# Kernel optimization log

Measured on AMD Instinct MI355X. Metric: run time of the kernel, lower is better.

The kernel has to match this reference:

```python
import jax, jax.numpy as jnp
import numpy as np

B, S, H, NH, L, ML = 4, 2048, 768, 8, 128, 15
DH = H // NH
PERIOD = 16  # newline every 16 tokens -> 15 content tokens per line


def _layernorm(x, g, b, eps=1e-5):
    m = x.mean(-1, keepdims=True)
    v = ((x - m) ** 2).mean(-1, keepdims=True)
    return (x - m) / jnp.sqrt(v + eps) * g + b


def setup_inputs() -> dict:
    key = jax.random.key(0)
    ks = jax.random.split(key, 8)
    sc = 0.02
    return {
        "hidden": jax.random.normal(ks[0], (B, S, H), jnp.float32),
        "in_proj_w": jax.random.normal(ks[1], (3 * H, H), jnp.float32) * sc,
        "in_proj_b": jnp.zeros((3 * H,), jnp.float32),
        "out_proj_w": jax.random.normal(ks[2], (H, H), jnp.float32) * sc,
        "out_proj_b": jnp.zeros((H,), jnp.float32),
        "W1": jax.random.normal(ks[3], (H, 2 * H), jnp.float32) * sc,
        "b1": jnp.zeros((H,), jnp.float32),
        "g1": jnp.ones((H,), jnp.float32),
        "be1": jnp.zeros((H,), jnp.float32),
        "W2": jax.random.normal(ks[4], (H, H), jnp.float32) * sc,
        "b2": jnp.zeros((H,), jnp.float32),
        "g2": jnp.ones((H,), jnp.float32),
        "be2": jnp.zeros((H,), jnp.float32),
        "W3": jax.random.normal(ks[5], (1, H), jnp.float32) * sc,
        "b3": jnp.zeros((1,), jnp.float32),
        # padded ragged line structure (what the torch loops derive from newline positions)
        "line_starts": jnp.tile(jnp.arange(L, dtype=jnp.int32) * PERIOD, (B, 1)),  # [B,L]
        "line_lens": jnp.full((B, L), ML, jnp.int32),                              # [B,L]
        "context_len": jnp.full((B,), S, jnp.int32),                               # [B]
    }


def reference(hidden, in_proj_w, in_proj_b, out_proj_w, out_proj_b,
              W1, b1, g1, be1, W2, b2, g2, be2, W3, b3,
              line_starts, line_lens, context_len):
    # --- gather per-line tokens into a padded [B, L, ML, H] block ---
    pos = line_starts[:, :, None] + jnp.arange(ML, dtype=line_starts.dtype)      # [B,L,ML]
    tok_mask = jnp.arange(ML)[None, None, :] < line_lens[:, :, None]             # [B,L,ML]
    pos_c = jnp.clip(pos, 0, S - 1)
    bidx = jnp.arange(B)[:, None, None]
    line_tok = hidden[bidx, pos_c]                                               # [B,L,ML,H]

    # --- nn.MultiheadAttention: query=line tokens, key/value=global context ---
    Wq, Wk, Wv = jnp.split(in_proj_w, 3, axis=0)
    bq, bk, bv = jnp.split(in_proj_b, 3, axis=0)
    q = (line_tok @ Wq.T + bq).reshape(B, L, ML, NH, DH)
    k = (hidden @ Wk.T + bk).reshape(B, S, NH, DH)
    v = (hidden @ Wv.T + bv).reshape(B, S, NH, DH)

    scale = 1.0 / np.float32(np.sqrt(DH))
    scores = jnp.einsum('blmhd,bshd->blhms', q, k) * scale                       # [B,L,NH,ML,S]
    kmask = jnp.arange(S)[None, :] < context_len[:, None]                        # [B,S]
    scores = jnp.where(kmask[:, None, None, None, :], scores, -1e9)
    attn = jax.nn.softmax(scores, axis=-1)
    o = jnp.einsum('blhms,bshd->blmhd', attn, v).reshape(B, L, ML, H)
    o = o @ out_proj_w.T + out_proj_b                                            # [B,L,ML,H]

    # --- masked mean-pool over the line's tokens ---
    m = tok_mask[..., None].astype(hidden.dtype)
    denom = jnp.maximum(line_lens, 1)[..., None].astype(hidden.dtype)            # [B,L,1]
    line_mean = (line_tok * m).sum(2) / denom                                    # [B,L,H]
    attn_mean = (o * m).sum(2) / denom                                           # [B,L,H]

    # --- classifier: Linear -> LN -> GELU -> Residual(Linear->LN->GELU) -> Linear ---
    x = jnp.concatenate([line_mean, attn_mean], axis=-1)                         # [B,L,2H]
    x = jax.nn.gelu(_layernorm(x @ W1.T + b1, g1, be1), approximate=False)
    x = x + jax.nn.gelu(_layernorm(x @ W2.T + b2, g2, be2), approximate=False)
    logits = (x @ W3.T + b3)[..., 0]                                             # [B,L]

    # empty lines get logit -10 (as in the torch loop)
    logits = jnp.where(line_lens > 0, logits, jnp.asarray(-10.0, logits.dtype))
    return jax.nn.sigmoid(logits)
```

## Files before the change

kernel.cpp:

```cpp
#include <hip/hip_runtime.h>
#include <hip/hip_bf16.h>
#include <cmath>

using bf16 = __hip_bfloat16;
typedef __attribute__((ext_vector_type(8))) short short8;
typedef __attribute__((ext_vector_type(4))) short s16x4;
typedef __attribute__((ext_vector_type(4))) float f32x4;

#define B_   4
#define S_   2048
#define H_   768
#define H2_  1536
#define H3_  2304
#define NH_  8
#define DH_  96
#define L_   128
#define ML_  15
#define LG_  8
#define QR_  128
#define CH_  32
#define NS_  2
#define SLC_ (S_ / NS_)
#define ELD  36
#define VTLD 56
#define KLD  104
#define VTR  112

__device__ __forceinline__ float gelu_exact(float v) {
    return 0.5f * v * (1.0f + erff(v * 0.7071067811865475f));
}
__device__ __forceinline__ short f2bs(float f) {
    bf16 h = __float2bfloat16(f);
    return *reinterpret_cast<short*>(&h);
}
__device__ __forceinline__ short8 ld_frag8(const short* p) {
    union { short8 v; s16x4 h[2]; } u;
    u.h[0] = *(const s16x4*)p;
    u.h[1] = *(const s16x4*)(p + 4);
    return u.v;
}

__global__ __launch_bounds__(256) void f2b_k(
    const float* __restrict__ src, bf16* __restrict__ dst, int n)
{
    const int i = (blockIdx.x * 256 + threadIdx.x) * 8;
    if (i >= n) return;
    float4 a = *(const float4*)(src + i);
    float4 b = *(const float4*)(src + i + 4);
    short8 r;
    r[0] = f2bs(a.x); r[1] = f2bs(a.y); r[2] = f2bs(a.z); r[3] = f2bs(a.w);
    r[4] = f2bs(b.x); r[5] = f2bs(b.y); r[6] = f2bs(b.z); r[7] = f2bs(b.w);
    *(short8*)(dst + i) = r;
}

template <typename T>
__device__ __forceinline__ void stage8(const T* src, bf16* dst);
template <>
__device__ __forceinline__ void stage8<bf16>(const bf16* src, bf16* dst) {
    *(int4*)dst = *(const int4*)src;
}
template <>
__device__ __forceinline__ void stage8<float>(const float* src, bf16* dst) {
    float4 a = *(const float4*)src;
    float4 b = *(const float4*)(src + 4);
    short8 r;
    r[0] = f2bs(a.x); r[1] = f2bs(a.y); r[2] = f2bs(a.z); r[3] = f2bs(a.w);
    r[4] = f2bs(b.x); r[5] = f2bs(b.y); r[6] = f2bs(b.z); r[7] = f2bs(b.w);
    *(short8*)dst = r;
}

__global__ __launch_bounds__(256) void gemm128_bt(
    const bf16* __restrict__ A, const bf16* __restrict__ Bm,
    const float* __restrict__ bias, bf16* __restrict__ C,
    int M, int N, int K, int ldc)
{
    __shared__ alignas(16) bf16 As[128 * 32];
    __shared__ alignas(16) bf16 Bs[128 * 32];
    const int t = threadIdx.x;
    const int wave = t >> 6, lane = t & 63;
    const int l15 = lane & 15, quad = lane >> 4;
    const int m0 = blockIdx.x * 128, n0 = blockIdx.y * 128;
    const int wm = wave & 1, wn = wave >> 1;
    const int srow = t >> 1, scol = (t & 1) * 16;

    const bf16* aP = A + (size_t)(m0 + srow) * K + scol;
    const bf16* bP = Bm + (size_t)(n0 + srow) * K + scol;
    bf16* aL = &As[srow * 32 + scol];
    bf16* bL = &Bs[srow * 32 + scol];

    f32x4 acc[4][4];
#pragma unroll
    for (int i = 0; i < 4; i++)
#pragma unroll
        for (int j = 0; j < 4; j++) acc[i][j] = (f32x4){0.f, 0.f, 0.f, 0.f};

    for (int k0 = 0; k0 < K; k0 += 32) {
        int4 ra0 = *(const int4*)(aP + k0);
        int4 ra1 = *(const int4*)(aP + k0 + 8);
        int4 rb0 = *(const int4*)(bP + k0);
        int4 rb1 = *(const int4*)(bP + k0 + 8);
        __syncthreads();
        *(int4*)aL = ra0; *(int4*)(aL + 8) = ra1;
        *(int4*)bL = rb0; *(int4*)(bL + 8) = rb1;
        __syncthreads();
        short8 af[4], bfq[4];
#pragma unroll
        for (int i = 0; i < 4; i++)
            af[i] = *(const short8*)&As[(wm * 64 + i * 16 + l15) * 32 + quad * 8];
#pragma unroll
        for (int j = 0; j < 4; j++)
            bfq[j] = *(const short8*)&Bs[(wn * 64 + j * 16 + l15) * 32 + quad * 8];
#pragma unroll
        for (int i = 0; i < 4; i++)
#pragma unroll
            for (int j = 0; j < 4; j++)
                acc[i][j] = __builtin_amdgcn_mfma_f32_16x16x32_bf16(af[i], bfq[j], acc[i][j], 0, 0, 0);
    }

#pragma unroll
    for (int j = 0; j < 4; j++) {
        const int col = n0 + wn * 64 + j * 16 + l15;
        const float bv = bias[col];
#pragma unroll
        for (int i = 0; i < 4; i++) {
            const int row = m0 + wm * 64 + i * 16 + quad * 4;
#pragma unroll
            for (int r = 0; r < 4; r++)
                C[(size_t)(row + r) * ldc + col] = __float2bfloat16(acc[i][j][r] + bv);
        }
    }
}

template <typename TA, typename TB, bool OUT_BF16>
__global__ __launch_bounds__(256) void gemm_bt(
    const TA* __restrict__ A, const TB* __restrict__ Bm,
    const float* __restrict__ bias, void* __restrict__ Cout,
    int M, int N, int K, int ldc, int coff)
{
    __shared__ alignas(16) bf16 As[64 * 32];
    __shared__ alignas(16) bf16 Bs[64 * 32];
    const int t = threadIdx.x;
    const int wave = t >> 6, lane = t & 63;
    const int l15 = lane & 15, quad = lane >> 4;
    const int m0 = blockIdx.x * 64, n0 = blockIdx.y * 64;
    const int srow = t >> 2, schk = (t & 3) * 8;

    const TA* aPtr = A + (size_t)(m0 + srow) * K + schk;
    const TB* bPtr = Bm + (size_t)(n0 + srow) * K + schk;

    f32x4 acc[4] = {{0.f,0.f,0.f,0.f},{0.f,0.f,0.f,0.f},
                    {0.f,0.f,0.f,0.f},{0.f,0.f,0.f,0.f}};
    const int aoff = (wave * 16 + l15) * 32 + quad * 8;

    for (int k0 = 0; k0 < K; k0 += 32) {
        __syncthreads();
        stage8<TA>(aPtr + k0, &As[srow * 32 + schk]);
        stage8<TB>(bPtr + k0, &Bs[srow * 32 + schk]);
        __syncthreads();
        short8 af = *(const short8*)&As[aoff];
#pragma unroll
        for (int nt = 0; nt < 4; nt++) {
            short8 bfr = *(const short8*)&Bs[(nt * 16 + l15) * 32 + quad * 8];
            acc[nt] = __builtin_amdgcn_mfma_f32_16x16x32_bf16(af, bfr, acc[nt], 0, 0, 0);
        }
    }

#pragma unroll
    for (int nt = 0; nt < 4; nt++) {
        int col = n0 + nt * 16 + l15;
        float bv = bias[col];
#pragma unroll
        for (int r = 0; r < 4; r++) {
            int row = m0 + wave * 16 + quad * 4 + r;
            float v = acc[nt][r] + bv;
            if (OUT_BF16) ((bf16*)Cout)[(size_t)row * ldc + coff + col] = __float2bfloat16(v);
            else          ((float*)Cout)[(size_t)row * ldc + coff + col] = v;
        }
    }
}

__global__ __launch_bounds__(256) void attn_slice(
    const bf16* __restrict__ qkv, const int* __restrict__ line_starts,
    const int* __restrict__ line_lens, const int* __restrict__ context_len,
    bf16* __restrict__ Opart, float* __restrict__ Dpart)
{
    __shared__ alignas(16) union {
        short Qs[QR_ * KLD];
        struct {
            short Ks[CH_ * KLD];
            short Vt[VTR * VTLD];
            short Es[QR_ * ELD];
        } s;
    } U;

    const int t = threadIdx.x;
    const int idx = blockIdx.x;
    const int slice = blockIdx.y;
    const int lg = idx & 15;
    const int bh = idx >> 4;
    const int h = bh & 7, b = bh >> 3;
    const int ctx = context_len[b];
    const int wave = t >> 6, lane = t & 63;
    const int l15 = lane & 15, quad = lane >> 4;

    for (int ii = t; ii < QR_ * 12; ii += 256) {
        const int r = ii / 12, ck = ii - r * 12;
        int4 val; val.x = val.y = val.z = val.w = 0;
        if (r < LG_ * ML_) {
            const int li = r / ML_, m = r - li * ML_;
            const int line = lg * LG_ + li;
            const int len = line_lens[b * L_ + line];
            if (m < len) {
                int sPos = line_starts[b * L_ + line] + m;
                sPos = min(max(sPos, 0), S_ - 1);
                val = *(const int4*)(qkv + (size_t)(b * S_ + sPos) * H3_ + h * DH_ + ck * 8);
            }
        }
        *(int4*)&U.Qs[r * KLD + ck * 8] = val;
    }
    __syncthreads();

    short8 qf[2][3];
#pragma unroll
    for (int st = 0; st < 2; st++)
#pragma unroll
        for (int kf = 0; kf < 3; kf++)
            qf[st][kf] = *(const short8*)(U.Qs + ((wave + 4 * st) * 16 + l15) * KLD + kf * 32 + quad * 8);
    __syncthreads();

    f32x4 Oacc[2][7];
#pragma unroll
    for (int st = 0; st < 2; st++)
#pragma unroll
        for (int nt = 0; nt < 7; nt++) Oacc[st][nt] = (f32x4){0.f, 0.f, 0.f, 0.f};

    const float scale = 0.10206207261596577f;
    const size_t kbase = (size_t)b * S_ * H3_ + H_ + h * DH_;
    const size_t vbase = kbase + H_;
    const int cbase = slice * SLC_;

    const int vt_qp = t / 12;
    const int vt_ck = t - vt_qp * 12;
    const int on_dd = t >> 4;
    const int on_sp = t & 15;

    int4 rk0, rk1; short8 rva, rvb;
    const int ki0 = 2 * t, ki1 = 2 * t + 1;
    if (t < 192) {
        rk0 = *(const int4*)(qkv + kbase + (size_t)(cbase + ki0 / 12) * H3_ + (ki0 % 12) * 8);
        rk1 = *(const int4*)(qkv + kbase + (size_t)(cbase + ki1 / 12) * H3_ + (ki1 % 12) * 8);
        const bf16* vs = qkv + vbase + (size_t)(cbase + 2 * vt_qp) * H3_ + vt_ck * 8;
        rva = *(const short8*)vs;
        rvb = *(const short8*)(vs + H3_);
    }

    for (int ci = 0; ci < SLC_ / CH_; ci++) {
        const int c0 = cbase + ci * CH_;
        __syncthreads();
        if (t < 192) {
            *(int4*)&U.s.Ks[(ki0 / 12) * KLD + (ki0 % 12) * 8] = rk0;
            *(int4*)&U.s.Ks[(ki1 / 12) * KLD + (ki1 % 12) * 8] = rk1;
#pragma unroll
            for (int j = 0; j < 8; j++) {
                unsigned int pk = (unsigned int)(unsigned short)rva[j]
                                | ((unsigned int)(unsigned short)rvb[j] << 16);
                *(unsigned int*)&U.s.Vt[(vt_ck * 8 + j) * VTLD + 2 * vt_qp] = pk;
            }
        }
        {
            unsigned int lo = (c0 + 2 * on_sp)     < ctx ? 0x3f80u : 0u;
            unsigned int hi = (c0 + 2 * on_sp + 1) < ctx ? 0x3f80u : 0u;
            *(unsigned int*)&U.s.Vt[(96 + on_dd) * VTLD + 2 * on_sp] = lo | (hi << 16);
        }
        __syncthreads();

        if (ci + 1 < SLC_ / CH_ && t < 192) {
            const int cn = c0 + CH_;
            rk0 = *(const int4*)(qkv + kbase + (size_t)(cn + ki0 / 12) * H3_ + (ki0 % 12) * 8);
            rk1 = *(const int4*)(qkv + kbase + (size_t)(cn + ki1 / 12) * H3_ + (ki1 % 12) * 8);
            const bf16* vs = qkv + vbase + (size_t)(cn + 2 * vt_qp) * H3_ + vt_ck * 8;
            rva = *(const short8*)vs;
            rvb = *(const short8*)(vs + H3_);
        }

        f32x4 acc[2][2] = {{{0.f,0.f,0.f,0.f},{0.f,0.f,0.f,0.f}},
                           {{0.f,0.f,0.f,0.f},{0.f,0.f,0.f,0.f}}};
#pragma unroll
        for (int ns = 0; ns < 2; ns++)
#pragma unroll
            for (int kf = 0; kf < 3; kf++) {
                short8 kfr = *(const short8*)(U.s.Ks + (ns * 16 + l15) * KLD + kf * 32 + quad * 8);
                acc[0][ns] = __builtin_amdgcn_mfma_f32_16x16x32_bf16(kfr, qf[0][kf], acc[0][ns], 0, 0, 0);
                acc[1][ns] = __builtin_amdgcn_mfma_f32_16x16x32_bf16(kfr, qf[1][kf], acc[1][ns], 0, 0, 0);
            }

#pragma unroll
        for (int st = 0; st < 2; st++)
#pragma unroll
            for (int ns = 0; ns < 2; ns++) {
                s16x4 wv;
#pragma unroll
                for (int r = 0; r < 4; r++) {
                    const int s = c0 + ns * 16 + quad * 4 + r;
                    float e = (s < ctx) ? __expf(acc[st][ns][r] * scale) : 0.f;
                    wv[r] = f2bs(e);
                }
                *(s16x4*)&U.s.Es[((wave + 4 * st) * 16 + l15) * ELD + ns * 16 + quad * 4] = wv;
            }

        short8 pf0 = ld_frag8(U.s.Es + (wave * 16 + l15) * ELD + quad * 8);
        short8 pf1 = ld_frag8(U.s.Es + ((wave + 4) * 16 + l15) * ELD + quad * 8);
#pragma unroll
        for (int nt = 0; nt < 7; nt++) {
            short8 vfr = *(const short8*)&U.s.Vt[(nt * 16 + l15) * VTLD + quad * 8];
            Oacc[0][nt] = __builtin_amdgcn_mfma_f32_16x16x32_bf16(pf0, vfr, Oacc[0][nt], 0, 0, 0);
            Oacc[1][nt] = __builtin_amdgcn_mfma_f32_16x16x32_bf16(pf1, vfr, Oacc[1][nt], 0, 0, 0);
        }
    }

    const size_t pb = (size_t)(slice * 512 + idx) * QR_;
#pragma unroll
    for (int st = 0; st < 2; st++)
#pragma unroll
        for (int r = 0; r < 4; r++) {
            const int row = (wave + 4 * st) * 16 + quad * 4 + r;
#pragma unroll
            for (int nt = 0; nt < 6; nt++)
                Opart[(pb + row) * DH_ + nt * 16 + l15] = __float2bfloat16(Oacc[st][nt][r]);
            if (l15 == 0) Dpart[pb + row] = Oacc[st][6][r];
        }
}

__global__ __launch_bounds__(256) void combine_pool(
    const bf16* __restrict__ Opart, const float* __restrict__ Dpart,
    const int* __restrict__ line_lens, bf16* __restrict__ opool)
{
    __shared__ float invd[LG_ * ML_];
    __shared__ int lens_s[LG_];
    const int idx = blockIdx.x;
    const int lg = idx & 15, bh = idx >> 4;
    const int h = bh & 7, b = bh >> 3;
    const int t = threadIdx.x;
    if (t < LG_) lens_s[t] = line_lens[b * L_ + lg * LG_ + t];
    if (t < LG_ * ML_) {
        float ds = 0.f;
#pragma unroll
        for (int s = 0; s < NS_; s++)
            ds += Dpart[(size_t)(s * 512 + idx) * QR_ + t];
        invd[t] = ds > 0.f ? 1.f / ds : 0.f;
    }
    __syncthreads();
    for (int q = t; q < LG_ * DH_; q += 256) {
        const int li = q / DH_, d = q - li * DH_;
        const int mm = min(lens_s[li], ML_);
        float acc = 0.f;
        for (int m = 0; m < mm; m++) {
            const int row = li * ML_ + m;
            float o = 0.f;
#pragma unroll
            for (int s = 0; s < NS_; s++)
                o += __bfloat162float(Opart[((size_t)(s * 512 + idx) * QR_ + row) * DH_ + d]);
            acc += o * invd[row];
        }
        const int line = lg * LG_ + li;
        opool[(size_t)(b * L_ + line) * H_ + h * DH_ + d] =
            __float2bfloat16(acc / (float)max(lens_s[li], 1));
    }
}

__global__ __launch_bounds__(256) void line_mean_k(
    const bf16* __restrict__ hidden, const int* __restrict__ line_starts,
    const int* __restrict__ line_lens, bf16* __restrict__ x)
{
    const int blk = blockIdx.x;
    const int b = blk >> 7, line = blk & 127;
    const int len = line_lens[b * L_ + line];
    const int start = line_starts[b * L_ + line];
    const int mm = min(len, ML_);
    const float inv = 1.f / (float)max(len, 1);
    for (int d = threadIdx.x; d < H_; d += 256) {
        float s = 0.f;
        for (int m = 0; m < mm; m++) {
            int sp = min(max(start + m, 0), S_ - 1);
            s += __bfloat162float(hidden[(size_t)(b * S_ + sp) * H_ + d]);
        }
        x[(size_t)blk * H2_ + d] = __float2bfloat16(s * inv);
    }
}

__global__ __launch_bounds__(256) void ln_gelu_k(
    const float* __restrict__ hin, const float* __restrict__ g,
    const float* __restrict__ be, float* __restrict__ uout, bf16* __restrict__ ubf)
{
    __shared__ float red[16];
    const int row = blockIdx.x, t = threadIdx.x;
    const float* hr = hin + (size_t)row * H_;
    float v[3];
    float s1 = 0.f, s2 = 0.f;
#pragma unroll
    for (int k = 0; k < 3; k++) {
        v[k] = hr[t + k * 256];
        s1 += v[k]; s2 += v[k] * v[k];
    }
#pragma unroll
    for (int m = 1; m < 64; m <<= 1) { s1 += __shfl_xor(s1, m, 64); s2 += __shfl_xor(s2, m, 64); }
    const int wave = t >> 6, lane = t & 63;
    if (lane == 0) { red[wave] = s1; red[8 + wave] = s2; }
    __syncthreads();
    s1 = red[0] + red[1] + red[2] + red[3];
    s2 = red[8] + red[9] + red[10] + red[11];
    const float mean = s1 * (1.f / H_);
    const float var = s2 * (1.f / H_) - mean * mean;
    const float rstd = 1.f / sqrtf(var + 1e-5f);
#pragma unroll
    for (int k = 0; k < 3; k++) {
        const int d = t + k * 256;
        float y = (v[k] - mean) * rstd * g[d] + be[d];
        y = gelu_exact(y);
        uout[(size_t)row * H_ + d] = y;
        ubf[(size_t)row * H_ + d] = __float2bfloat16(y);
    }
}

__global__ __launch_bounds__(256) void final_k(
    const float* __restrict__ h2, const float* __restrict__ u,
    const float* __restrict__ g2, const float* __restrict__ be2,
    const float* __restrict__ W3, const float* __restrict__ b3,
    const int* __restrict__ line_lens, float* __restrict__ out)
{
    __shared__ float red[16];
    const int row = blockIdx.x, t = threadIdx.x;
    const float* hr = h2 + (size_t)row * H_;
    float v[3];
    float s1 = 0.f, s2 = 0.f;
#pragma unroll
    for (int k = 0; k < 3; k++) {
        v[k] = hr[t + k * 256];
        s1 += v[k]; s2 += v[k] * v[k];
    }
#pragma unroll
    for (int m = 1; m < 64; m <<= 1) { s1 += __shfl_xor(s1, m, 64); s2 += __shfl_xor(s2, m, 64); }
    const int wave = t >> 6, lane = t & 63;
    if (lane == 0) { red[wave] = s1; red[8 + wave] = s2; }
    __syncthreads();
    s1 = red[0] + red[1] + red[2] + red[3];
    s2 = red[8] + red[9] + red[10] + red[11];
    const float mean = s1 * (1.f / H_);
    const float var = s2 * (1.f / H_) - mean * mean;
    const float rstd = 1.f / sqrtf(var + 1e-5f);
    float dotp = 0.f;
#pragma unroll
    for (int k = 0; k < 3; k++) {
        const int d = t + k * 256;
        float y = (v[k] - mean) * rstd * g2[d] + be2[d];
        y = u[(size_t)row * H_ + d] + gelu_exact(y);
        dotp += y * W3[d];
    }
#pragma unroll
    for (int m = 1; m < 64; m <<= 1) dotp += __shfl_xor(dotp, m, 64);
    __syncthreads();
    if (lane == 0) red[wave] = dotp;
    __syncthreads();
    if (t == 0) {
        float logit = red[0] + red[1] + red[2] + red[3] + b3[0];
        if (line_lens[row] <= 0) logit = -10.f;
        out[row] = 1.f / (1.f + __expf(-logit));
    }
}

extern "C" void kernel_launch(void* const* d_in, const int* in_sizes, int n_in,
                              void* d_out, int out_size, void* d_ws, size_t ws_size,
                              hipStream_t stream)
{
    const float* hidden     = (const float*)d_in[0];
    const float* in_proj_w  = (const float*)d_in[1];
    const float* in_proj_b  = (const float*)d_in[2];
    const float* out_proj_w = (const float*)d_in[3];
    const float* out_proj_b = (const float*)d_in[4];
    const float* W1         = (const float*)d_in[5];
    const float* b1         = (const float*)d_in[6];
    const float* g1         = (const float*)d_in[7];
    const float* be1        = (const float*)d_in[8];
    const float* W2         = (const float*)d_in[9];
    const float* b2         = (const float*)d_in[10];
    const float* g2         = (const float*)d_in[11];
    const float* be2        = (const float*)d_in[12];
    const float* W3         = (const float*)d_in[13];
    const float* b3         = (const float*)d_in[14];
    const int* line_starts  = (const int*)d_in[15];
    const int* line_lens    = (const int*)d_in[16];
    const int* context_len  = (const int*)d_in[17];

    const int BL = B_ * L_;
    const size_t nh = (size_t)B_ * S_ * H_;
    const size_t nw = (size_t)H3_ * H_;
    const size_t opart_n = (size_t)NS_ * 512 * QR_ * DH_;

    char* w = (char*)d_ws;
    bf16* qkv   = (bf16*)w;  w += (size_t)B_ * S_ * H3_ * sizeof(bf16);
    char* ovl = w;
    bf16* hb    = (bf16*)ovl;
    bf16* wqkvb = (bf16*)(ovl + nh * sizeof(bf16));
    bf16* Opart = (bf16*)ovl;
    w = ovl + opart_n * sizeof(bf16);
    float* Dpart = (float*)w; w += (size_t)NS_ * 512 * QR_ * sizeof(float);
    bf16* opool = (bf16*)w;  w += (size_t)BL * H_ * sizeof(bf16);
    bf16* x     = (bf16*)w;  w += (size_t)BL * H2_ * sizeof(bf16);
    float* h1   = (float*)w; w += (size_t)BL * H_ * sizeof(float);
    float* uu   = (float*)w; w += (size_t)BL * H_ * sizeof(float);
    bf16* ubf   = (bf16*)w;  w += (size_t)BL * H_ * sizeof(bf16);
    float* h2   = (float*)w; w += (size_t)BL * H_ * sizeof(float);

    f2b_k<<<(int)(nh / (256 * 8)), 256, 0, stream>>>(hidden, hb, (int)nh);
    f2b_k<<<(int)(nw / (256 * 8)), 256, 0, stream>>>(in_proj_w, wqkvb, (int)nw);

    gemm128_bt<<<dim3(B_ * S_ / 128, H3_ / 128), 256, 0, stream>>>(
        hb, wqkvb, in_proj_b, qkv, B_ * S_, H3_, H_, H3_);
    line_mean_k<<<BL, 256, 0, stream>>>(hb, line_starts, line_lens, x);
    attn_slice<<<dim3(512, NS_), 256, 0, stream>>>(
        qkv, line_starts, line_lens, context_len, Opart, Dpart);
    combine_pool<<<512, 256, 0, stream>>>(Opart, Dpart, line_lens, opool);
    gemm_bt<bf16, float, true><<<dim3(BL / 64, H_ / 64), 256, 0, stream>>>(
        opool, out_proj_w, out_proj_b, x, BL, H_, H_, H2_, H_);
    gemm_bt<bf16, float, false><<<dim3(BL / 64, H_ / 64), 256, 0, stream>>>(
        x, W1, b1, h1, BL, H_, H2_, H_, 0);
    ln_gelu_k<<<BL, 256, 0, stream>>>(h1, g1, be1, uu, ubf);
    gemm_bt<bf16, float, false><<<dim3(BL / 64, H_ / 64), 256, 0, stream>>>(
        ubf, W2, b2, h2, BL, H_, H_, H_, 0);
    final_k<<<BL, 256, 0, stream>>>(h2, uu, g2, be2, W3, b3, line_lens, (float*)d_out);
}
```

Before: 370.7 us.

## Write V pre-transposed from QKV GEMM epilogue and stage it directly in attention

The QKV projection epilogue now splits its output: Q/K go to a compact [B,S,2H] buffer and V is written transposed per head as [B,NH,DH,S]. The attention kernel then loads V^T tiles with contiguous 16-byte reads straight into shared memory instead of transposing V element-pairs in registers, and all 256 threads take part in staging. The V^T shared row stride shrinks. The cost is strided 8-byte scatter stores in the GEMM epilogue for the V third of the output.

```diff
diff --git a/kernel.cpp b/kernel.cpp
--- a/kernel.cpp
+++ b/kernel.cpp
@@ -22,7 +22,7 @@
 #define NS_  2
 #define SLC_ (S_ / NS_)
 #define ELD  36
-#define VTLD 56
+#define VTLD 40
 #define KLD  104
 #define VTR  112
 
@@ -69,10 +69,10 @@
     *(short8*)dst = r;
 }
 
-__global__ __launch_bounds__(256) void gemm128_bt(
+__global__ __launch_bounds__(256) void gemm128_qkv(
     const bf16* __restrict__ A, const bf16* __restrict__ Bm,
-    const float* __restrict__ bias, bf16* __restrict__ C,
-    int M, int N, int K, int ldc)
+    const float* __restrict__ bias, bf16* __restrict__ qk,
+    bf16* __restrict__ vt, int M, int K)
 {
     __shared__ alignas(16) bf16 As[128 * 32];
     __shared__ alignas(16) bf16 Bs[128 * 32];
@@ -117,16 +117,35 @@
                 acc[i][j] = __builtin_amdgcn_mfma_f32_16x16x32_bf16(af[i], bfq[j], acc[i][j], 0, 0, 0);
     }
 
-#pragma unroll
-    for (int j = 0; j < 4; j++) {
-        const int col = n0 + wn * 64 + j * 16 + l15;
-        const float bv = bias[col];
-#pragma unroll
-        for (int i = 0; i < 4; i++) {
-            const int row = m0 + wm * 64 + i * 16 + quad * 4;
-#pragma unroll
-            for (int r = 0; r < 4; r++)
-                C[(size_t)(row + r) * ldc + col] = __float2bfloat16(acc[i][j][r] + bv);
+    if (n0 < H2_) {
+#pragma unroll
+        for (int j = 0; j < 4; j++) {
+            const int col = n0 + wn * 64 + j * 16 + l15;
+            const float bv = bias[col];
+#pragma unroll
+            for (int i = 0; i < 4; i++) {
+                const int row = m0 + wm * 64 + i * 16 + quad * 4;
+#pragma unroll
+                for (int r = 0; r < 4; r++)
+                    qk[(size_t)(row + r) * H2_ + col] = __float2bfloat16(acc[i][j][r] + bv);
+            }
+        }
+    } else {
+#pragma unroll
+        for (int j = 0; j < 4; j++) {
+            const int col = n0 + wn * 64 + j * 16 + l15;
+            const float bv = bias[col];
+            const int dfull = col - H2_;
+            const int hh = dfull / DH_, d = dfull - hh * DH_;
+#pragma unroll
+            for (int i = 0; i < 4; i++) {
+                const int row = m0 + wm * 64 + i * 16 + quad * 4;
+                const int b = row >> 11, s = row & (S_ - 1);
+                s16x4 pk;
+#pragma unroll
+                for (int r = 0; r < 4; r++) pk[r] = f2bs(acc[i][j][r] + bv);
+                *(s16x4*)&vt[((size_t)(b * NH_ + hh) * DH_ + d) * S_ + s] = pk;
+            }
         }
     }
 }
@@ -180,8 +199,9 @@
 }
 
 __global__ __launch_bounds__(256) void attn_slice(
-    const bf16* __restrict__ qkv, const int* __restrict__ line_starts,
-    const int* __restrict__ line_lens, const int* __restrict__ context_len,
+    const bf16* __restrict__ qk, const bf16* __restrict__ vtg,
+    const int* __restrict__ line_starts, const int* __restrict__ line_lens,
+    const int* __restrict__ context_len,
     bf16* __restrict__ Opart, float* __restrict__ Dpart)
 {
     __shared__ alignas(16) union {
@@ -213,7 +233,7 @@
             if (m < len) {
                 int sPos = line_starts[b * L_ + line] + m;
                 sPos = min(max(sPos, 0), S_ - 1);
-                val = *(const int4*)(qkv + (size_t)(b * S_ + sPos) * H3_ + h * DH_ + ck * 8);
+                val = *(const int4*)(qk + (size_t)(b * S_ + sPos) * H2_ + h * DH_ + ck * 8);
             }
         }
         *(int4*)&U.Qs[r * KLD + ck * 8] = val;
@@ -235,52 +255,50 @@
         for (int nt = 0; nt < 7; nt++) Oacc[st][nt] = (f32x4){0.f, 0.f, 0.f, 0.f};
 
     const float scale = 0.10206207261596577f;
-    const size_t kbase = (size_t)b * S_ * H3_ + H_ + h * DH_;
-    const size_t vbase = kbase + H_;
+    const size_t kbase = (size_t)b * S_ * H2_ + H_ + h * DH_;
+    const size_t vbase = (size_t)(b * NH_ + h) * DH_ * S_;
     const int cbase = slice * SLC_;
 
-    const int vt_qp = t / 12;
-    const int vt_ck = t - vt_qp * 12;
-    const int on_dd = t >> 4;
-    const int on_sp = t & 15;
-
-    int4 rk0, rk1; short8 rva, rvb;
-    const int ki0 = 2 * t, ki1 = 2 * t + 1;
-    if (t < 192) {
-        rk0 = *(const int4*)(qkv + kbase + (size_t)(cbase + ki0 / 12) * H3_ + (ki0 % 12) * 8);
-        rk1 = *(const int4*)(qkv + kbase + (size_t)(cbase + ki1 / 12) * H3_ + (ki1 % 12) * 8);
-        const bf16* vs = qkv + vbase + (size_t)(cbase + 2 * vt_qp) * H3_ + vt_ck * 8;
-        rva = *(const short8*)vs;
-        rvb = *(const short8*)(vs + H3_);
+    const int k0r = t / 12,        k0c = t - k0r * 12;
+    const int k1r = (256 + t) / 12, k1c = (256 + t) - k1r * 12;
+    const int v0d = t >> 2,        v0s = (t & 3) * 8;
+    const int v1d = (256 + t) >> 2, v1s = ((256 + t) & 3) * 8;
+    const int on_r = t >> 4, on_c = t & 15;
+
+    int4 rk0, rk1, rv0, rv1;
+    {
+        rk0 = *(const int4*)(qk + kbase + (size_t)(cbase + k0r) * H2_ + k0c * 8);
+        rv0 = *(const int4*)(vtg + vbase + (size_t)v0d * S_ + cbase + v0s);
+        if (t < 128) {
+            rk1 = *(const int4*)(qk + kbase + (size_t)(cbase + k1r) * H2_ + k1c * 8);
+            rv1 = *(const int4*)(vtg + vbase + (size_t)v1d * S_ + cbase + v1s);
+        }
     }
 
     for (int ci = 0; ci < SLC_ / CH_; ci++) {
         const int c0 = cbase + ci * CH_;
         __syncthreads();
-        if (t < 192) {
-            *(int4*)&U.s.Ks[(ki0 / 12) * KLD + (ki0 % 12) * 8] = rk0;
-            *(int4*)&U.s.Ks[(ki1 / 12) * KLD + (ki1 % 12) * 8] = rk1;
-#pragma unroll
-            for (int j = 0; j < 8; j++) {
-                unsigned int pk = (unsigned int)(unsigned short)rva[j]
-                                | ((unsigned int)(unsigned short)rvb[j] << 16);
-                *(unsigned int*)&U.s.Vt[(vt_ck * 8 + j) * VTLD + 2 * vt_qp] = pk;
+        *(int4*)&U.s.Ks[k0r * KLD + k0c * 8] = rk0;
+        *(int4*)&U.s.Vt[v0d * VTLD + v0s] = rv0;
+        if (t < 128) {
+            *(int4*)&U.s.Ks[k1r * KLD + k1c * 8] = rk1;
+            *(int4*)&U.s.Vt[v1d * VTLD + v1s] = rv1;
+        }
+        {
+            unsigned int lo = (c0 + 2 * on_c)     < ctx ? 0x3f80u : 0u;
+            unsigned int hi = (c0 + 2 * on_c + 1) < ctx ? 0x3f80u : 0u;
+            ((unsigned int*)&U.s.Vt[(96 + on_r) * VTLD])[on_c] = lo | (hi << 16);
+        }
+        __syncthreads();
+
+        if (ci + 1 < SLC_ / CH_) {
+            const int cn = c0 + CH_;
+            rk0 = *(const int4*)(qk + kbase + (size_t)(cn + k0r) * H2_ + k0c * 8);
+            rv0 = *(const int4*)(vtg + vbase + (size_t)v0d * S_ + cn + v0s);
+            if (t < 128) {
+                rk1 = *(const int4*)(qk + kbase + (size_t)(cn + k1r) * H2_ + k1c * 8);
+                rv1 = *(const int4*)(vtg + vbase + (size_t)v1d * S_ + cn + v1s);
             }
-        }
-        {
-            unsigned int lo = (c0 + 2 * on_sp)     < ctx ? 0x3f80u : 0u;
-            unsigned int hi = (c0 + 2 * on_sp + 1) < ctx ? 0x3f80u : 0u;
-            *(unsigned int*)&U.s.Vt[(96 + on_dd) * VTLD + 2 * on_sp] = lo | (hi << 16);
-        }
-        __syncthreads();
-
-        if (ci + 1 < SLC_ / CH_ && t < 192) {
-            const int cn = c0 + CH_;
-            rk0 = *(const int4*)(qkv + kbase + (size_t)(cn + ki0 / 12) * H3_ + (ki0 % 12) * 8);
-            rk1 = *(const int4*)(qkv + kbase + (size_t)(cn + ki1 / 12) * H3_ + (ki1 % 12) * 8);
-            const bf16* vs = qkv + vbase + (size_t)(cn + 2 * vt_qp) * H3_ + vt_ck * 8;
-            rva = *(const short8*)vs;
-            rvb = *(const short8*)(vs + H3_);
         }
 
         f32x4 acc[2][2] = {{{0.f,0.f,0.f,0.f},{0.f,0.f,0.f,0.f}},
@@ -497,7 +515,8 @@
     const size_t opart_n = (size_t)NS_ * 512 * QR_ * DH_;
 
     char* w = (char*)d_ws;
-    bf16* qkv   = (bf16*)w;  w += (size_t)B_ * S_ * H3_ * sizeof(bf16);
+    bf16* qk    = (bf16*)w;  w += (size_t)B_ * S_ * H2_ * sizeof(bf16);
+    bf16* vtg   = (bf16*)w;  w += (size_t)B_ * NH_ * DH_ * S_ * sizeof(bf16);
     char* ovl = w;
     bf16* hb    = (bf16*)ovl;
     bf16* wqkvb = (bf16*)(ovl + nh * sizeof(bf16));
@@ -514,11 +533,11 @@
     f2b_k<<<(int)(nh / (256 * 8)), 256, 0, stream>>>(hidden, hb, (int)nh);
     f2b_k<<<(int)(nw / (256 * 8)), 256, 0, stream>>>(in_proj_w, wqkvb, (int)nw);
 
-    gemm128_bt<<<dim3(B_ * S_ / 128, H3_ / 128), 256, 0, stream>>>(
-        hb, wqkvb, in_proj_b, qkv, B_ * S_, H3_, H_, H3_);
+    gemm128_qkv<<<dim3(B_ * S_ / 128, H3_ / 128), 256, 0, stream>>>(
+        hb, wqkvb, in_proj_b, qk, vtg, B_ * S_, H_);
     line_mean_k<<<BL, 256, 0, stream>>>(hb, line_starts, line_lens, x);
     attn_slice<<<dim3(512, NS_), 256, 0, stream>>>(
-        qkv, line_starts, line_lens, context_len, Opart, Dpart);
+        qk, vtg, line_starts, line_lens, context_len, Opart, Dpart);
     combine_pool<<<512, 256, 0, stream>>>(Opart, Dpart, line_lens, opool);
     gemm_bt<bf16, float, true><<<dim3(BL / 64, H_ / 64), 256, 0, stream>>>(
         opool, out_proj_w, out_proj_b, x, BL, H_, H_, H2_, H_);
```

Result: faster. 348.3 us (-6.0%).
